# Optimization experiments

Hardware: AMD Instinct MI355X
Metric: run time of the kernel (lower is better)

Reference implementation:

```python
import jax, jax.numpy as jnp
import numpy as np

B, C, H, W = 8, 32, 512, 512
BN_EPS = 1e-5


def setup_inputs() -> dict:
    key = jax.random.key(0)
    k1, k2, k3, k4 = jax.random.split(key, 4)
    x = jax.random.normal(k1, (B, C, H, W), dtype=jnp.float32)
    # 1x1 conv weight: [out=4, in=4*C] (kaiming-like scale)
    w_compress = jax.random.normal(k2, (4, 4 * C), dtype=jnp.float32) / np.sqrt(4 * C)
    gamma = jnp.ones((4,), dtype=jnp.float32)
    beta = jnp.zeros((4,), dtype=jnp.float32)
    return {"x": x, "w_compress": w_compress, "gamma": gamma, "beta": beta}


def _four_dir(x):
    # zero-pad H and W by 1; shifted view at (di, dj) gives x[i+di, j+dj]
    xp = jnp.pad(x, ((0, 0), (0, 0), (1, 1), (1, 1)))

    def sh(di, dj):
        return jax.lax.dynamic_slice(xp, (0, 0, 1 + di, 1 + dj), x.shape)

    # PyTorch conv = cross-correlation: kernel one at (r,c) reads x[i+r-1, j+c-1]
    ne = sh(-1, +1) - x
    nw = sh(-1, -1) - x
    se = sh(+1, +1) - x
    sw = sh(+1, -1) - x
    return jnp.concatenate([ne, nw, se, sw], axis=1)  # [B, 4C, H, W]


def reference(x, w_compress, gamma, beta):
    feat = _four_dir(x)
    # 1x1 conv: channel mixing 4C -> 4
    y = jnp.einsum("oc,bchw->bohw", w_compress, feat)
    # BatchNorm2d (training mode: batch statistics, biased variance)
    mean = jnp.mean(y, axis=(0, 2, 3), keepdims=True)
    var = jnp.var(y, axis=(0, 2, 3), keepdims=True)
    y_hat = (y - mean) * jax.lax.rsqrt(var + BN_EPS)
    return y_hat * gamma[None, :, None, None] + beta[None, :, None, None]
```

## Files before the change

### kernel.cpp

```cpp
#include <hip/hip_runtime.h>

#define B_ 8
#define C_ 32
#define H_ 512
#define W_ 512
#define HW_ (H_ * W_)
#define BN_EPS 1e-5f

typedef float f4v __attribute__((ext_vector_type(4)));


__global__ __launch_bounds__(256, 2) void fourdir_compute(
    const float* __restrict__ x,
    const float* __restrict__ w,
    float* __restrict__ y,
    float* __restrict__ sums)
{
    __shared__ f4v wl4[5][C_];
    const int t = threadIdx.x;
    {
        float* wl = (float*)wl4;
        for (int idx = t; idx < 4 * 4 * C_; idx += 256) {
            int o  = idx & 3;
            int dc = idx >> 2;
            wl[idx] = w[o * (4 * C_) + dc];
        }
    }
    __syncthreads();
    if (t < 4 * C_) {
        float* wl = (float*)wl4;
        wl[512 + t] = -(wl[t] + wl[128 + t] + wl[256 + t] + wl[384 + t]);
    }
    __syncthreads();

    const int lane = t & 63;
    const int wv   = t >> 6;
    const int cg   = lane & 15;
    const int sr   = lane >> 4;
    const int j0 = (blockIdx.x << 6) + (cg << 2);
    const int i0 = (blockIdx.y << 6) + (wv << 4) + (sr << 2);
    const int b  = blockIdx.z;
    const float* xb = x + (size_t)b * C_ * HW_;

    const bool jm = (j0 > 0);
    const bool jp = (j0 + 4 < W_);
    const bool tv = (i0 > 0);
    const bool bv = (i0 + 4 < H_);

    int off[6];
    {
        const int rows[6] = { tv ? i0 - 1 : 0, i0, i0 + 1, i0 + 2, i0 + 3,
                              bv ? i0 + 4 : H_ - 1 };
#pragma unroll
        for (int k = 0; k < 6; ++k) off[k] = rows[k] * W_ + j0;
    }

    f4v acc[4][4];
#pragma unroll
    for (int p = 0; p < 4; ++p)
#pragma unroll
        for (int q = 0; q < 4; ++q) acc[p][q] = f4v{0.f, 0.f, 0.f, 0.f};

#pragma unroll 2
    for (int c = 0; c < C_; ++c) {
        const float* xc = xb + (size_t)c * HW_;
        f4v  vr[6];
        float lf[6], rt[6];
#pragma unroll
        for (int k = 0; k < 6; ++k) {
            vr[k] = *(const f4v*)(xc + off[k]);
            lf[k] = jm ? xc[off[k] - 1] : 0.f;
            rt[k] = jp ? xc[off[k] + 4] : 0.f;
        }
        if (!tv) { vr[0] = f4v{0.f,0.f,0.f,0.f}; lf[0] = 0.f; rt[0] = 0.f; }
        if (!bv) { vr[5] = f4v{0.f,0.f,0.f,0.f}; lf[5] = 0.f; rt[5] = 0.f; }

        const f4v wne = wl4[0][c];
        const f4v wnw = wl4[1][c];
        const f4v wse = wl4[2][c];
        const f4v wsw = wl4[3][c];
        const f4v wct = wl4[4][c];

#pragma unroll
        for (int p = 0; p < 4; ++p) {
#pragma unroll
            for (int q = 0; q < 4; ++q) {
                const float ne = (q < 3) ? vr[p][q + 1]     : rt[p];
                const float nw = (q > 0) ? vr[p][q - 1]     : lf[p];
                const float se = (q < 3) ? vr[p + 2][q + 1] : rt[p + 2];
                const float sw = (q > 0) ? vr[p + 2][q - 1] : lf[p + 2];
                const float ct = vr[p + 1][q];
                acc[p][q] += wne * ne + wnw * nw + wse * se + wsw * sw + wct * ct;
            }
        }
    }

#pragma unroll
    for (int p = 0; p < 4; ++p) {
        const size_t base = (size_t)(i0 + p) * W_ + j0;
#pragma unroll
        for (int o = 0; o < 4; ++o) {
            f4v st = { acc[p][0][o], acc[p][1][o], acc[p][2][o], acc[p][3][o] };
            *(f4v*)(y + ((size_t)(b * 4 + o)) * HW_ + base) = st;
        }
    }

    f4v s0 = f4v{0.f,0.f,0.f,0.f}, s1 = f4v{0.f,0.f,0.f,0.f};
#pragma unroll
    for (int p = 0; p < 4; ++p)
#pragma unroll
        for (int q = 0; q < 4; ++q) {
            s0 += acc[p][q];
            s1 += acc[p][q] * acc[p][q];
        }

    float vals[8] = { s0[0], s0[1], s0[2], s0[3], s1[0], s1[1], s1[2], s1[3] };
#pragma unroll
    for (int k = 0; k < 8; ++k) {
        float v = vals[k];
#pragma unroll
        for (int o = 32; o >= 1; o >>= 1) v += __shfl_xor(v, o, 64);
        vals[k] = v;
    }

    __shared__ float red[4][8];
    if (lane == 0) {
#pragma unroll
        for (int k = 0; k < 8; ++k) red[wv][k] = vals[k];
    }
    __syncthreads();
    if (t < 8) {
        const float s = red[0][t] + red[1][t] + red[2][t] + red[3][t];
        atomicAdd(&sums[t], s);
    }
}

__global__ __launch_bounds__(256) void bn_norm(
    float* __restrict__ y,
    const float* __restrict__ sums,
    const float* __restrict__ gamma,
    const float* __restrict__ beta)
{
    const int gid = blockIdx.x * 256 + threadIdx.x;
    const size_t base = (size_t)gid * 4;
    const int o = (int)((base / HW_) & 3);

    const float n = (float)((size_t)B_ * HW_);
    const float mean  = sums[o] / n;
    const float var   = sums[4 + o] / n - mean * mean;
    const float scale = rsqrtf(var + BN_EPS) * gamma[o];
    const float shift = beta[o] - mean * scale;

    float4 v = *(const float4*)(y + base);
    v.x = v.x * scale + shift;
    v.y = v.y * scale + shift;
    v.z = v.z * scale + shift;
    v.w = v.w * scale + shift;
    *(float4*)(y + base) = v;
}

extern "C" void kernel_launch(void* const* d_in, const int* in_sizes, int n_in,
                              void* d_out, int out_size, void* d_ws, size_t ws_size,
                              hipStream_t stream) {
    const float* x     = (const float*)d_in[0];
    const float* w     = (const float*)d_in[1];
    const float* gamma = (const float*)d_in[2];
    const float* beta  = (const float*)d_in[3];
    float* out  = (float*)d_out;
    float* sums = (float*)d_ws;

    hipMemsetAsync(sums, 0, 8 * sizeof(float), stream);

    dim3 gridA(W_ / 64, H_ / 64, B_);
    fourdir_compute<<<gridA, 256, 0, stream>>>(x, w, out, sums);

    const int nf4 = (B_ * 4 * HW_) / 4;
    bn_norm<<<nf4 / 256, 256, 0, stream>>>(out, sums, gamma, beta);
}
```

Baseline: 394.4 us.

## Shrink per-thread tile to 2 rows and software-pipeline channel loads

```diff
diff --git a/kernel.cpp b/kernel.cpp
--- a/kernel.cpp
+++ b/kernel.cpp
@@ -10,7 +10,51 @@
 typedef float f4v __attribute__((ext_vector_type(4)));
 
 
-__global__ __launch_bounds__(256, 2) void fourdir_compute(
+__device__ __forceinline__ void loadch(
+    const float* __restrict__ xc, const int off[4],
+    const int loff[4], const int roff[4],
+    bool jm, bool jp, bool tv, bool bv,
+    f4v vr[4], float lf[4], float rt[4])
+{
+#pragma unroll
+    for (int k = 0; k < 4; ++k) {
+        vr[k] = *(const f4v*)(xc + off[k]);
+        lf[k] = xc[loff[k]];
+        rt[k] = xc[roff[k]];
+    }
+#pragma unroll
+    for (int k = 0; k < 4; ++k) {
+        if (!jm) lf[k] = 0.f;
+        if (!jp) rt[k] = 0.f;
+    }
+    if (!tv) { vr[0] = f4v{0.f,0.f,0.f,0.f}; lf[0] = 0.f; rt[0] = 0.f; }
+    if (!bv) { vr[3] = f4v{0.f,0.f,0.f,0.f}; lf[3] = 0.f; rt[3] = 0.f; }
+}
+
+__device__ __forceinline__ void fmach(
+    const f4v (*__restrict__ wl4)[C_], int c,
+    const f4v vr[4], const float lf[4], const float rt[4],
+    f4v acc[2][4])
+{
+    const f4v wne = wl4[0][c];
+    const f4v wnw = wl4[1][c];
+    const f4v wse = wl4[2][c];
+    const f4v wsw = wl4[3][c];
+    const f4v wct = wl4[4][c];
+#pragma unroll
+    for (int p = 0; p < 2; ++p)
+#pragma unroll
+        for (int q = 0; q < 4; ++q) {
+            const float ne = (q < 3) ? vr[p][q + 1]     : rt[p];
+            const float nw = (q > 0) ? vr[p][q - 1]     : lf[p];
+            const float se = (q < 3) ? vr[p + 2][q + 1] : rt[p + 2];
+            const float sw = (q > 0) ? vr[p + 2][q - 1] : lf[p + 2];
+            const float ct = vr[p + 1][q];
+            acc[p][q] += wne * ne + wnw * nw + wse * se + wsw * sw + wct * ct;
+        }
+}
+
+__global__ __launch_bounds__(256, 4) void fourdir_compute(
     const float* __restrict__ x,
     const float* __restrict__ w,
     float* __restrict__ y,
@@ -20,83 +64,65 @@
     const int t = threadIdx.x;
     {
         float* wl = (float*)wl4;
-        for (int idx = t; idx < 4 * 4 * C_; idx += 256) {
+        for (int idx = t; idx < 512; idx += 256) {
             int o  = idx & 3;
             int dc = idx >> 2;
-            wl[idx] = w[o * (4 * C_) + dc];
+            wl[idx] = w[o * 128 + dc];
         }
     }
     __syncthreads();
-    if (t < 4 * C_) {
+    if (t < 128) {
         float* wl = (float*)wl4;
         wl[512 + t] = -(wl[t] + wl[128 + t] + wl[256 + t] + wl[384 + t]);
     }
     __syncthreads();
 
-    const int lane = t & 63;
-    const int wv   = t >> 6;
-    const int cg   = lane & 15;
-    const int sr   = lane >> 4;
+    const int cg = t & 15;
+    const int rp = t >> 4;
     const int j0 = (blockIdx.x << 6) + (cg << 2);
-    const int i0 = (blockIdx.y << 6) + (wv << 4) + (sr << 2);
+    const int i0 = (blockIdx.y << 5) + (rp << 1);
     const int b  = blockIdx.z;
     const float* xb = x + (size_t)b * C_ * HW_;
 
     const bool jm = (j0 > 0);
     const bool jp = (j0 + 4 < W_);
     const bool tv = (i0 > 0);
-    const bool bv = (i0 + 4 < H_);
-
-    int off[6];
+    const bool bv = (i0 + 2 < H_);
+
+    int off[4], loff[4], roff[4];
     {
-        const int rows[6] = { tv ? i0 - 1 : 0, i0, i0 + 1, i0 + 2, i0 + 3,
-                              bv ? i0 + 4 : H_ - 1 };
-#pragma unroll
-        for (int k = 0; k < 6; ++k) off[k] = rows[k] * W_ + j0;
-    }
-
-    f4v acc[4][4];
-#pragma unroll
-    for (int p = 0; p < 4; ++p)
+        const int rows[4] = { tv ? i0 - 1 : 0, i0, i0 + 1, bv ? i0 + 2 : H_ - 1 };
+#pragma unroll
+        for (int k = 0; k < 4; ++k) {
+            off[k]  = rows[k] * W_ + j0;
+            loff[k] = off[k] - (jm ? 1 : 0);
+            roff[k] = off[k] + (jp ? 4 : 3);
+        }
+    }
+
+    f4v acc[2][4];
+#pragma unroll
+    for (int p = 0; p < 2; ++p)
 #pragma unroll
         for (int q = 0; q < 4; ++q) acc[p][q] = f4v{0.f, 0.f, 0.f, 0.f};
 
-#pragma unroll 2
-    for (int c = 0; c < C_; ++c) {
-        const float* xc = xb + (size_t)c * HW_;
-        f4v  vr[6];
-        float lf[6], rt[6];
-#pragma unroll
-        for (int k = 0; k < 6; ++k) {
-            vr[k] = *(const f4v*)(xc + off[k]);
-            lf[k] = jm ? xc[off[k] - 1] : 0.f;
-            rt[k] = jp ? xc[off[k] + 4] : 0.f;
-        }
-        if (!tv) { vr[0] = f4v{0.f,0.f,0.f,0.f}; lf[0] = 0.f; rt[0] = 0.f; }
-        if (!bv) { vr[5] = f4v{0.f,0.f,0.f,0.f}; lf[5] = 0.f; rt[5] = 0.f; }
-
-        const f4v wne = wl4[0][c];
-        const f4v wnw = wl4[1][c];
-        const f4v wse = wl4[2][c];
-        const f4v wsw = wl4[3][c];
-        const f4v wct = wl4[4][c];
-
-#pragma unroll
-        for (int p = 0; p < 4; ++p) {
-#pragma unroll
-            for (int q = 0; q < 4; ++q) {
-                const float ne = (q < 3) ? vr[p][q + 1]     : rt[p];
-                const float nw = (q > 0) ? vr[p][q - 1]     : lf[p];
-                const float se = (q < 3) ? vr[p + 2][q + 1] : rt[p + 2];
-                const float sw = (q > 0) ? vr[p + 2][q - 1] : lf[p + 2];
-                const float ct = vr[p + 1][q];
-                acc[p][q] += wne * ne + wnw * nw + wse * se + wsw * sw + wct * ct;
-            }
-        }
-    }
-
-#pragma unroll
-    for (int p = 0; p < 4; ++p) {
+    f4v vrA[4], vrB[4];
+    float lfA[4], rtA[4], lfB[4], rtB[4];
+
+    loadch(xb, off, loff, roff, jm, jp, tv, bv, vrA, lfA, rtA);
+#pragma unroll 1
+    for (int c = 0; c < C_ - 2; c += 2) {
+        loadch(xb + (size_t)(c + 1) * HW_, off, loff, roff, jm, jp, tv, bv, vrB, lfB, rtB);
+        fmach(wl4, c, vrA, lfA, rtA, acc);
+        loadch(xb + (size_t)(c + 2) * HW_, off, loff, roff, jm, jp, tv, bv, vrA, lfA, rtA);
+        fmach(wl4, c + 1, vrB, lfB, rtB, acc);
+    }
+    loadch(xb + (size_t)(C_ - 1) * HW_, off, loff, roff, jm, jp, tv, bv, vrB, lfB, rtB);
+    fmach(wl4, C_ - 2, vrA, lfA, rtA, acc);
+    fmach(wl4, C_ - 1, vrB, lfB, rtB, acc);
+
+#pragma unroll
+    for (int p = 0; p < 2; ++p) {
         const size_t base = (size_t)(i0 + p) * W_ + j0;
 #pragma unroll
         for (int o = 0; o < 4; ++o) {
@@ -107,7 +133,7 @@
 
     f4v s0 = f4v{0.f,0.f,0.f,0.f}, s1 = f4v{0.f,0.f,0.f,0.f};
 #pragma unroll
-    for (int p = 0; p < 4; ++p)
+    for (int p = 0; p < 2; ++p)
 #pragma unroll
         for (int q = 0; q < 4; ++q) {
             s0 += acc[p][q];
@@ -124,6 +150,8 @@
     }
 
     __shared__ float red[4][8];
+    const int wv   = t >> 6;
+    const int lane = t & 63;
     if (lane == 0) {
 #pragma unroll
         for (int k = 0; k < 8; ++k) red[wv][k] = vals[k];
@@ -171,7 +199,7 @@
 
     hipMemsetAsync(sums, 0, 8 * sizeof(float), stream);
 
-    dim3 gridA(W_ / 64, H_ / 64, B_);
+    dim3 gridA(W_ / 64, H_ / 32, B_);
     fourdir_compute<<<gridA, 256, 0, stream>>>(x, w, out, sums);
 
     const int nf4 = (B_ * 4 * HW_) / 4;
```

Result: slower. 785.1 us (+99.1%).
